# Performance work log

Hardware: AMD Instinct MI355X
Metric: run time of the kernel (lower is better)

Reference implementation:

```python
import jax, jax.numpy as jnp
import numpy as np

BETA = 0.25


def setup_inputs() -> dict:
    key = jax.random.key(0)
    k1, k2 = jax.random.split(key)
    B, D, H, W, K = 16, 256, 32, 32, 8192
    z_e = jax.random.normal(k1, (B, D, H, W), dtype=jnp.float32)
    # codebook init uniform(-1/K, 1/K) as in torch
    codebook = jax.random.uniform(k2, (K, D), dtype=jnp.float32,
                                  minval=-1.0 / K, maxval=1.0 / K)
    return {"z_e": z_e, "codebook": codebook}


def reference(z_e, codebook):
    B, D, H, W = z_e.shape
    K = codebook.shape[0]
    # (B, D, H, W) -> (BHW, D)
    z_flat = jnp.transpose(z_e, (0, 2, 3, 1)).reshape(-1, D)

    # distances computed under no_grad in torch -> stop_gradient here
    zf = jax.lax.stop_gradient(z_flat)
    cb = jax.lax.stop_gradient(codebook)
    # ||z||^2 + ||e||^2 - 2 z.e  -> (BHW, K)
    dist = ((zf * zf).sum(axis=1, keepdims=True)
            + (cb * cb).sum(axis=1)[None, :]
            - 2.0 * (zf @ cb.T))
    indices = jnp.argmin(dist, axis=1)  # (BHW,)

    # embedding gather, reshape back to (B, D, H, W)
    z_q_flat = codebook[indices]
    z_q = jnp.transpose(z_q_flat.reshape(B, H, W, D), (0, 3, 1, 2))

    # straight-through estimator
    z_q_st = z_e + jax.lax.stop_gradient(z_q - z_e)

    codebook_loss = jnp.mean((jax.lax.stop_gradient(z_q) - z_e) ** 2)
    commitment_loss = jnp.mean((z_q - jax.lax.stop_gradient(z_e)) ** 2)
    vq_loss = codebook_loss + BETA * commitment_loss

    # perplexity: one_hot(indices).mean(0) == counts / N
    N = z_flat.shape[0]
    counts = jnp.zeros((K,), dtype=z_flat.dtype).at[indices].add(1.0)
    avg_probs = counts / N
    perplexity = jnp.exp(-jnp.sum(avg_probs * jnp.log(avg_probs + 1e-10)))

    return (z_q_st, vq_loss, indices.reshape(B, H, W), perplexity)
```

## Files before the change

### kernel.cpp

```cpp
#include <hip/hip_runtime.h>

#define DD 256
#define KK 8192
#define HW 1024
#define NROWS 16384
#define NELEM 4194304
#define MT 32
#define MS 64
#define MARGIN 6e-4f
#define WCAP 1024
#define NSLICE 4

typedef __attribute__((ext_vector_type(8))) short short8;
typedef __attribute__((ext_vector_type(4))) float f32x4;
typedef __attribute__((ext_vector_type(4))) unsigned int ux4;
typedef unsigned short ushort;
typedef unsigned int uint;
typedef unsigned long long u64;

__device__ __forceinline__ float np_pw128_sq(const float* p) {
  float r[8];
#pragma unroll
  for (int j = 0; j < 8; ++j) r[j] = __fmul_rn(p[j], p[j]);
  for (int i = 8; i < 128; i += 8) {
#pragma unroll
    for (int j = 0; j < 8; ++j)
      r[j] = __fadd_rn(r[j], __fmul_rn(p[i + j], p[i + j]));
  }
  return __fadd_rn(__fadd_rn(__fadd_rn(r[0], r[1]), __fadd_rn(r[2], r[3])),
                   __fadd_rn(__fadd_rn(r[4], r[5]), __fadd_rn(r[6], r[7])));
}

__device__ __forceinline__ ushort f2bf(float x) {
  uint u = __float_as_uint(x);
  u += 0x7FFF + ((u >> 16) & 1);
  return (ushort)(u >> 16);
}

__device__ __forceinline__ uint fenc(float f) {
  uint u = __float_as_uint(f);
  return (u & 0x80000000u) ? ~u : (u | 0x80000000u);
}
__device__ __forceinline__ float fdec(uint k) {
  return __uint_as_float((k & 0x80000000u) ? (k & 0x7FFFFFFFu) : ~k);
}

struct Top2 { float m1, m2; int i1; };

__device__ __forceinline__ void top2_upd(Top2& s, const f32x4 a,
                                         const f32x4 Bs, int ibase) {
  float d0 = fmaf(-2.f, a[0], Bs[0]);
  float d1 = fmaf(-2.f, a[1], Bs[1]);
  float d2 = fmaf(-2.f, a[2], Bs[2]);
  float d3 = fmaf(-2.f, a[3], Bs[3]);
  float lo01 = fminf(d0, d1), hi01 = fmaxf(d0, d1);
  int io01 = d1 < d0 ? ibase + 1 : ibase;
  float lo23 = fminf(d2, d3), hi23 = fmaxf(d2, d3);
  int io23 = d3 < d2 ? ibase + 3 : ibase + 2;
  float n1 = fminf(lo01, lo23);
  int ni = lo23 < lo01 ? io23 : io01;
  float n2 = fminf(fmaxf(lo01, lo23), fminf(hi01, hi23));
  s.m2 = fminf(fmaxf(s.m1, n1), fminf(s.m2, n2));
  s.i1 = n1 < s.m1 ? ni : s.i1;
  s.m1 = fminf(s.m1, n1);
}

__device__ __forceinline__ void top2_bfly(Top2& s, int off) {
  float om1 = __shfl_xor(s.m1, off);
  int oi1 = __shfl_xor(s.i1, off);
  float om2 = __shfl_xor(s.m2, off);
  s.m2 = fminf(fmaxf(s.m1, om1), fminf(s.m2, om2));
  s.i1 = om1 < s.m1 ? oi1 : s.i1;
  s.m1 = fminf(s.m1, om1);
}

__device__ __forceinline__ uint pack_m2(float m2, int i1) {
  uint u = __float_as_uint(m2);
  uint hi = u & 0xFFFF0000u;
  if ((u & 0x80000000u) && (u & 0xFFFFu)) hi += 0x10000u;
  return hi | (uint)i1;
}

__global__ __launch_bounds__(256) void vq_prep(const float* __restrict__ cb,
                                               float* __restrict__ Bk,
                                               ushort* __restrict__ cbB) {
  const int b = blockIdx.x, t = threadIdx.x;
  if (b < 64) {
    int tid2 = b * 256 + t;
    int k = tid2 >> 1, half = tid2 & 1;
    float h = np_pw128_sq(cb + (size_t)k * DD + half * 128);
    float ho = __shfl_xor(h, 1);
    if (half == 0) Bk[k] = __fadd_rn(h, ho);
  } else {
    int tid = (b - 64) * 256 + t;
    int g = tid >> 9, s = (tid >> 6) & 7, lane = tid & 63;
    int code = g * 16 + (lane & 15);
    int dbase = s * 32 + (lane >> 4) * 8;
    const float* p = cb + (size_t)code * DD + dbase;
    ushort bb[8];
#pragma unroll
    for (int j = 0; j < 8; ++j) bb[j] = f2bf(p[j]);
    uint4 pk;
    pk.x = bb[0] | ((uint)bb[1] << 16);
    pk.y = bb[2] | ((uint)bb[3] << 16);
    pk.z = bb[4] | ((uint)bb[5] << 16);
    pk.w = bb[6] | ((uint)bb[7] << 16);
    *(uint4*)(cbB + (size_t)tid * 8) = pk;
  }
}

#define GG_BODY(BUF, GGI, IB)                                                  \
  {                                                                            \
    f32x4 A0 = {0,0,0,0}, A1 = {0,0,0,0}, A2 = {0,0,0,0}, A3 = {0,0,0,0};      \
    _Pragma("unroll")                                                          \
    for (int s = 0; s < 8; ++s) {                                              \
      A0 = __builtin_amdgcn_mfma_f32_16x16x32_bf16(BUF[s], aF0[s], A0, 0, 0, 0);\
      A1 = __builtin_amdgcn_mfma_f32_16x16x32_bf16(BUF[s], aF1[s], A1, 0, 0, 0);\
      A2 = __builtin_amdgcn_mfma_f32_16x16x32_bf16(BUF[s], aF2[s], A2, 0, 0, 0);\
      A3 = __builtin_amdgcn_mfma_f32_16x16x32_bf16(BUF[s], aF3[s], A3, 0, 0, 0);\
    }                                                                          \
    const f32x4 Bs = *(const f32x4*)(BkS + (GGI) * 16 - cbase + quad * 4);     \
    top2_upd(c0, A0, Bs, IB); top2_upd(c1, A1, Bs, IB);                        \
    top2_upd(c2, A2, Bs, IB); top2_upd(c3, A3, Bs, IB);                        \
  }

__global__ __launch_bounds__(256, 1) void vq_screen(
    const float* __restrict__ z, const ushort* __restrict__ cbB,
    const float* __restrict__ Bk, float* __restrict__ tA,
    uint* __restrict__ tB, uint* __restrict__ rowMinG) {
  __shared__ ushort ztB[MS][264];
  __shared__ float BkS[2048];
  const int bid = blockIdx.x;
  const int rt = bid >> 2, cs = bid & 3;
  const int t = threadIdx.x;
  const int n0 = rt * MS;
  const int bimg = n0 >> 10, hw0 = n0 & 1023;
  const float* zb = z + (size_t)bimg * DD * HW + hw0;

  for (int li = t; li < MS * 128; li += 256) {
    int r = li & 63, dp = li >> 6;
    float v0 = zb[(size_t)(2 * dp) * HW + r];
    float v1 = zb[(size_t)(2 * dp + 1) * HW + r];
    *(uint*)&ztB[r][2 * dp] = (uint)f2bf(v0) | ((uint)f2bf(v1) << 16);
  }
  for (int li = t; li < 2048; li += 256) BkS[li] = Bk[cs * 2048 + li];
  __syncthreads();

  const int w = t >> 6, lane = t & 63;
  const int quad = lane >> 4, n16 = lane & 15;

  short8 aF0[8], aF1[8], aF2[8], aF3[8];
#pragma unroll
  for (int s = 0; s < 8; ++s) {
    aF0[s] = *(const short8*)&ztB[n16][s * 32 + quad * 8];
    aF1[s] = *(const short8*)&ztB[16 + n16][s * 32 + quad * 8];
    aF2[s] = *(const short8*)&ztB[32 + n16][s * 32 + quad * 8];
    aF3[s] = *(const short8*)&ztB[48 + n16][s * 32 + quad * 8];
  }
#pragma unroll
  for (int s = 0; s < 8; ++s) {
    asm volatile("" : "+v"(*(ux4*)&aF0[s]));
    asm volatile("" : "+v"(*(ux4*)&aF1[s]));
    asm volatile("" : "+v"(*(ux4*)&aF2[s]));
    asm volatile("" : "+v"(*(ux4*)&aF3[s]));
  }

  const int gg0 = cs * 128 + w * 32;
  const int cbase = cs * 2048;
  Top2 c0 = {3.4e38f, 3.4e38f, 0}, c1 = {3.4e38f, 3.4e38f, 0};
  Top2 c2 = {3.4e38f, 3.4e38f, 0}, c3 = {3.4e38f, 3.4e38f, 0};
  float rmin = 3.4e38f;

  short8 b0[8], b1[8];
  {
    const ushort* bp = cbB + (size_t)gg0 * 4096 + lane * 8;
#pragma unroll
    for (int s = 0; s < 8; ++s) b0[s] = *(const short8*)(bp + s * 512);
  }

  for (int gp = 0; gp < 16; ++gp) {
    const int gg = gg0 + gp * 2;
    {
      const ushort* bp = cbB + (size_t)(gg + 1) * 4096 + lane * 8;
#pragma unroll
      for (int s = 0; s < 8; ++s) b1[s] = *(const short8*)(bp + s * 512);
    }
    GG_BODY(b0, gg, quad * 4)
    if (gp < 15) {
      const ushort* bp = cbB + (size_t)(gg + 2) * 4096 + lane * 8;
#pragma unroll
      for (int s = 0; s < 8; ++s) b0[s] = *(const short8*)(bp + s * 512);
    }
    GG_BODY(b1, gg + 1, 16 + quad * 4)
    top2_bfly(c0, 16); top2_bfly(c0, 32);
    top2_bfly(c1, 16); top2_bfly(c1, 32);
    top2_bfly(c2, 16); top2_bfly(c2, 32);
    top2_bfly(c3, 16); top2_bfly(c3, 32);
    const size_t tbase = (size_t)(gg >> 1) * NROWS + n0;
    if (quad == 0) {
      __builtin_nontemporal_store(c0.m1, &tA[tbase + n16]);
      __builtin_nontemporal_store(pack_m2(c0.m2, c0.i1), &tB[tbase + n16]);
      rmin = fminf(rmin, c0.m1);
    } else if (quad == 1) {
      __builtin_nontemporal_store(c1.m1, &tA[tbase + 16 + n16]);
      __builtin_nontemporal_store(pack_m2(c1.m2, c1.i1), &tB[tbase + 16 + n16]);
      rmin = fminf(rmin, c1.m1);
    } else if (quad == 2) {
      __builtin_nontemporal_store(c2.m1, &tA[tbase + 32 + n16]);
      __builtin_nontemporal_store(pack_m2(c2.m2, c2.i1), &tB[tbase + 32 + n16]);
      rmin = fminf(rmin, c2.m1);
    } else {
      __builtin_nontemporal_store(c3.m1, &tA[tbase + 48 + n16]);
      __builtin_nontemporal_store(pack_m2(c3.m2, c3.i1), &tB[tbase + 48 + n16]);
      rmin = fminf(rmin, c3.m1);
    }
    c0 = Top2{3.4e38f, 3.4e38f, 0}; c1 = Top2{3.4e38f, 3.4e38f, 0};
    c2 = Top2{3.4e38f, 3.4e38f, 0}; c3 = Top2{3.4e38f, 3.4e38f, 0};
  }
  atomicMin(&rowMinG[n0 + quad * 16 + n16], fenc(rmin));
}

__global__ __launch_bounds__(256) void vq_rerank(
    const float* __restrict__ z, const float* __restrict__ cb,
    const float* __restrict__ Bk, const float* __restrict__ tA,
    const uint* __restrict__ tB, const uint* __restrict__ rowMinG,
    float* __restrict__ out, int* __restrict__ hist,
    float* __restrict__ loss_acc, u64* __restrict__ rowBest) {
  __shared__ float zt[MT][DD + 1];
  __shared__ float thr[MT];
  __shared__ float ArS[MT];
  __shared__ int wl[WCAP];
  __shared__ int wcnt;
  __shared__ int kwin[MT];
  __shared__ float lred[4];

  const int t = threadIdx.x;
  const int n0 = blockIdx.x * MT;
  const int bimg = n0 >> 10, hw0 = n0 & 1023;
  const float* zb = z + (size_t)bimg * DD * HW + hw0;

  if (t == 0) wcnt = 0;
  for (int li = t; li < MT * DD; li += 256) {
    int d = li >> 5, r = li & 31;
    zt[r][d] = zb[d * HW + r];
  }
  __syncthreads();

  const int w = t >> 6, lane = t & 63;

  if (t < MT) {
    thr[t] = fdec(rowMinG[n0 + t]) + MARGIN;
  } else if (t >= 128 && t < 192) {
    int rr = (t - 128) >> 1, half = t & 1;
    float h = np_pw128_sq(&zt[rr][half * 128]);
    float ho = __shfl_xor(h, 1);
    if (half == 0) ArS[rr] = __fadd_rn(h, ho);
  }
  __syncthreads();

  auto exact_one = [&](int rr, int code) {
    const float* cp = cb + (size_t)code * DD;
    float dot = 0.f;
#pragma unroll
    for (int d0 = 0; d0 < DD; d0 += 4) {
      float4 v = *(const float4*)(cp + d0);
      dot = fmaf(zt[rr][d0 + 0], v.x, dot);
      dot = fmaf(zt[rr][d0 + 1], v.y, dot);
      dot = fmaf(zt[rr][d0 + 2], v.z, dot);
      dot = fmaf(zt[rr][d0 + 3], v.w, dot);
    }
    float bd = __fsub_rn(__fadd_rn(ArS[rr], Bk[code]), __fmul_rn(2.f, dot));
    atomicMin(&rowBest[n0 + rr],
              ((u64)__float_as_uint(bd) << 32) | (unsigned)code);
  };

  for (int it = 0; it < 8; ++it) {
    const int li = it * 256 + t;
    const int tile = li >> 3, r4 = (li & 7) << 2;
    const f32x4 a4 = __builtin_nontemporal_load(
        (const f32x4*)&tA[(size_t)tile * NROWS + n0 + r4]);
#pragma unroll
    for (int e = 0; e < 4; ++e) {
      const int rr = r4 + e;
      const float th = thr[rr];
      if (a4[e] <= th) {
        const uint pk = __builtin_nontemporal_load(
            &tB[(size_t)tile * NROWS + n0 + rr]);
        const float m2f = __uint_as_float(pk & 0xFFFF0000u);
        if (m2f <= th) {
          for (int c = 0; c < 32; ++c) {
            int pos = atomicAdd(&wcnt, 1);
            if (pos < WCAP) wl[pos] = (rr << 16) | (tile * 32 + c);
            else exact_one(rr, tile * 32 + c);
          }
        } else {
          int pos = atomicAdd(&wcnt, 1);
          if (pos < WCAP) wl[pos] = (rr << 16) | (tile * 32 + (int)(pk & 31u));
          else exact_one(rr, tile * 32 + (int)(pk & 31u));
        }
      }
    }
  }
  __syncthreads();

  const int cnt = min(wcnt, WCAP);
  for (int e = t; e < cnt; e += 256) {
    const int ent = wl[e];
    exact_one(ent >> 16, ent & 0xFFFF);
  }
  __syncthreads();

  if (t < MT) {
    u64 key = atomicMin(&rowBest[n0 + t], 0xFFFFFFFFFFFFFFFFull);
    int bi = (int)(key & 0xFFFFFFFFull);
    kwin[t] = bi;
    atomicAdd(&hist[bi], 1);
    out[(size_t)NELEM + 1 + n0 + t] = (float)bi;
  }
  __syncthreads();

  float lsum = 0.f;
  for (int it = 0; it < MT * DD / 256; ++it) {
    int li = it * 256 + t;
    int d = li >> 5, rr = li & 31;
    float ze = zt[rr][d];
    float zq = cb[(size_t)kwin[rr] * DD + d];
    float diff = __fsub_rn(zq, ze);
    float st = __fadd_rn(ze, diff);
    out[(size_t)(bimg * DD + d) * HW + hw0 + rr] = st;
    lsum = fmaf(diff, diff, lsum);
  }
#pragma unroll
  for (int off = 32; off > 0; off >>= 1) lsum += __shfl_down(lsum, off);
  if (lane == 0) lred[w] = lsum;
  __syncthreads();
  if (t == 0)
    atomicAdd(loss_acc, ((lred[0] + lred[1]) + (lred[2] + lred[3])));
}

__global__ __launch_bounds__(256) void vq_final(const int* __restrict__ hist,
                                                const float* __restrict__ loss,
                                                float* __restrict__ out) {
  __shared__ float sred[256];
  int t = threadIdx.x;
  float s = 0.f;
  for (int k = t; k < KK; k += 256) {
    float p = (float)hist[k] * (1.f / 16384.f);
    s += p * logf(p + 1e-10f);
  }
  sred[t] = s;
  __syncthreads();
  for (int off = 128; off > 0; off >>= 1) {
    if (t < off) sred[t] += sred[t + off];
    __syncthreads();
  }
  if (t == 0) {
    float L = loss[0] / (float)NELEM;
    out[NELEM] = 1.25f * L;
    out[(size_t)NELEM + 1 + NROWS] = expf(-sred[0]);
  }
}

extern "C" void kernel_launch(void* const* d_in, const int* in_sizes, int n_in,
                              void* d_out, int out_size, void* d_ws, size_t ws_size,
                              hipStream_t stream) {
  const float* z = (const float*)d_in[0];
  const float* cb = (const float*)d_in[1];
  float* out = (float*)d_out;

  float* wsf = (float*)d_ws;
  int* hist = (int*)d_ws;
  float* loss = wsf + 8192;
  float* Bk = wsf + 8448;
  uint* rowMinG = (uint*)(wsf + 16640);
  u64* rowBest = (u64*)(wsf + 33024);
  ushort* cbB = (ushort*)(wsf + 65792);
  float* tA = wsf + 1114368;
  uint* tB = (uint*)(wsf + 5308672);

  hipMemsetAsync(d_ws, 0, 8448 * sizeof(float), stream);
  hipMemsetAsync(wsf + 16640, 0xFF, 196608, stream);
  vq_prep<<<1088, 256, 0, stream>>>(cb, Bk, cbB);
  vq_screen<<<(NROWS / MS) * NSLICE, 256, 0, stream>>>(z, cbB, Bk, tA, tB,
                                                       rowMinG);
  vq_rerank<<<NROWS / MT, 256, 0, stream>>>(z, cb, Bk, tA, tB, rowMinG, out,
                                            hist, loss, rowBest);
  vq_final<<<1, 256, 0, stream>>>(hist, loss, out);
}
```

Before: 221.3 us.

## Fold workspace memsets into prep kernel and keep per-row best in LDS

```diff
diff --git a/kernel.cpp b/kernel.cpp
--- a/kernel.cpp
+++ b/kernel.cpp
@@ -83,7 +83,10 @@
 
 __global__ __launch_bounds__(256) void vq_prep(const float* __restrict__ cb,
                                                float* __restrict__ Bk,
-                                               ushort* __restrict__ cbB) {
+                                               ushort* __restrict__ cbB,
+                                               uint* __restrict__ rowMinG,
+                                               int* __restrict__ hist,
+                                               float* __restrict__ loss) {
   const int b = blockIdx.x, t = threadIdx.x;
   if (b < 64) {
     int tid2 = b * 256 + t;
@@ -91,6 +94,9 @@
     float h = np_pw128_sq(cb + (size_t)k * DD + half * 128);
     float ho = __shfl_xor(h, 1);
     if (half == 0) Bk[k] = __fadd_rn(h, ho);
+    rowMinG[tid2] = 0xFFFFFFFFu;
+    if (b < 32) hist[tid2] = 0;
+    if (tid2 == 0) loss[0] = 0.f;
   } else {
     int tid = (b - 64) * 256 + t;
     int g = tid >> 9, s = (tid >> 6) & 7, lane = tid & 63;
@@ -124,7 +130,8 @@
     top2_upd(c2, A2, Bs, IB); top2_upd(c3, A3, Bs, IB);                        \
   }
 
-__global__ __launch_bounds__(256, 1) void vq_screen(
+__global__ __launch_bounds__(256)
+__attribute__((amdgpu_waves_per_eu(1, 2))) void vq_screen(
     const float* __restrict__ z, const ushort* __restrict__ cbB,
     const float* __restrict__ Bk, float* __restrict__ tA,
     uint* __restrict__ tB, uint* __restrict__ rowMinG) {
@@ -225,12 +232,13 @@
     const float* __restrict__ Bk, const float* __restrict__ tA,
     const uint* __restrict__ tB, const uint* __restrict__ rowMinG,
     float* __restrict__ out, int* __restrict__ hist,
-    float* __restrict__ loss_acc, u64* __restrict__ rowBest) {
+    float* __restrict__ loss_acc) {
   __shared__ float zt[MT][DD + 1];
-  __shared__ float thr[MT];
   __shared__ float ArS[MT];
   __shared__ int wl[WCAP];
   __shared__ int wcnt;
+  __shared__ int ovf;
+  __shared__ u64 rowBestS[MT];
   __shared__ int kwin[MT];
   __shared__ float lred[4];
 
@@ -239,18 +247,56 @@
   const int bimg = n0 >> 10, hw0 = n0 & 1023;
   const float* zb = z + (size_t)bimg * DD * HW + hw0;
 
-  if (t == 0) wcnt = 0;
-  for (int li = t; li < MT * DD; li += 256) {
-    int d = li >> 5, r = li & 31;
-    zt[r][d] = zb[d * HW + r];
-  }
-  __syncthreads();
-
-  const int w = t >> 6, lane = t & 63;
-
-  if (t < MT) {
-    thr[t] = fdec(rowMinG[n0 + t]) + MARGIN;
-  } else if (t >= 128 && t < 192) {
+  if (t == 0) { wcnt = 0; ovf = 0; }
+  if (t < MT) rowBestS[t] = 0xFFFFFFFFFFFFFFFFull;
+  __syncthreads();
+
+  const int r4 = (t & 7) << 2;
+  float th[4];
+#pragma unroll
+  for (int e = 0; e < 4; ++e) th[e] = fdec(rowMinG[n0 + r4 + e]) + MARGIN;
+
+  float zv[32];
+#pragma unroll
+  for (int it = 0; it < 32; ++it) {
+    int li = it * 256 + t;
+    zv[it] = zb[(size_t)(li >> 5) * HW + (li & 31)];
+  }
+
+  for (int it = 0; it < 8; ++it) {
+    const int li = it * 256 + t;
+    const int tile = li >> 3;
+    const f32x4 a4 = __builtin_nontemporal_load(
+        (const f32x4*)&tA[(size_t)tile * NROWS + n0 + r4]);
+#pragma unroll
+    for (int e = 0; e < 4; ++e) {
+      if (a4[e] <= th[e]) {
+        const int rr = r4 + e;
+        const uint pk = __builtin_nontemporal_load(
+            &tB[(size_t)tile * NROWS + n0 + rr]);
+        const float m2f = __uint_as_float(pk & 0xFFFF0000u);
+        if (m2f <= th[e]) {
+          for (int c = 0; c < 32; ++c) {
+            int pos = atomicAdd(&wcnt, 1);
+            if (pos < WCAP) wl[pos] = (rr << 16) | (tile * 32 + c);
+            else ovf = 1;
+          }
+        } else {
+          int pos = atomicAdd(&wcnt, 1);
+          if (pos < WCAP) wl[pos] = (rr << 16) | (tile * 32 + (int)(pk & 31u));
+          else ovf = 1;
+        }
+      }
+    }
+  }
+
+#pragma unroll
+  for (int it = 0; it < 32; ++it) {
+    int li = it * 256 + t;
+    zt[li & 31][li >> 5] = zv[it];
+  }
+  __syncthreads();
+  if (t >= 128 && t < 192) {
     int rr = (t - 128) >> 1, half = t & 1;
     float h = np_pw128_sq(&zt[rr][half * 128]);
     float ho = __shfl_xor(h, 1);
@@ -270,49 +316,39 @@
       dot = fmaf(zt[rr][d0 + 3], v.w, dot);
     }
     float bd = __fsub_rn(__fadd_rn(ArS[rr], Bk[code]), __fmul_rn(2.f, dot));
-    atomicMin(&rowBest[n0 + rr],
-              ((u64)__float_as_uint(bd) << 32) | (unsigned)code);
+    atomicMin(&rowBestS[rr], ((u64)__float_as_uint(bd) << 32) | (unsigned)code);
   };
-
-  for (int it = 0; it < 8; ++it) {
-    const int li = it * 256 + t;
-    const int tile = li >> 3, r4 = (li & 7) << 2;
-    const f32x4 a4 = __builtin_nontemporal_load(
-        (const f32x4*)&tA[(size_t)tile * NROWS + n0 + r4]);
-#pragma unroll
-    for (int e = 0; e < 4; ++e) {
-      const int rr = r4 + e;
-      const float th = thr[rr];
-      if (a4[e] <= th) {
-        const uint pk = __builtin_nontemporal_load(
-            &tB[(size_t)tile * NROWS + n0 + rr]);
-        const float m2f = __uint_as_float(pk & 0xFFFF0000u);
-        if (m2f <= th) {
-          for (int c = 0; c < 32; ++c) {
-            int pos = atomicAdd(&wcnt, 1);
-            if (pos < WCAP) wl[pos] = (rr << 16) | (tile * 32 + c);
-            else exact_one(rr, tile * 32 + c);
-          }
-        } else {
-          int pos = atomicAdd(&wcnt, 1);
-          if (pos < WCAP) wl[pos] = (rr << 16) | (tile * 32 + (int)(pk & 31u));
-          else exact_one(rr, tile * 32 + (int)(pk & 31u));
-        }
-      }
-    }
-  }
-  __syncthreads();
 
   const int cnt = min(wcnt, WCAP);
   for (int e = t; e < cnt; e += 256) {
     const int ent = wl[e];
     exact_one(ent >> 16, ent & 0xFFFF);
   }
-  __syncthreads();
-
+  if (ovf) {
+    for (int it = 0; it < 8; ++it) {
+      const int li = it * 256 + t;
+      const int tile = li >> 3;
+      const f32x4 a4 = *(const f32x4*)&tA[(size_t)tile * NROWS + n0 + r4];
+#pragma unroll
+      for (int e = 0; e < 4; ++e) {
+        if (a4[e] <= th[e]) {
+          const int rr = r4 + e;
+          const uint pk = tB[(size_t)tile * NROWS + n0 + rr];
+          const float m2f = __uint_as_float(pk & 0xFFFF0000u);
+          if (m2f <= th[e]) {
+            for (int c = 0; c < 32; ++c) exact_one(rr, tile * 32 + c);
+          } else {
+            exact_one(rr, tile * 32 + (int)(pk & 31u));
+          }
+        }
+      }
+    }
+  }
+  __syncthreads();
+
+  const int w = t >> 6, lane = t & 63;
   if (t < MT) {
-    u64 key = atomicMin(&rowBest[n0 + t], 0xFFFFFFFFFFFFFFFFull);
-    int bi = (int)(key & 0xFFFFFFFFull);
+    int bi = (int)(rowBestS[t] & 0xFFFFFFFFull);
     kwin[t] = bi;
     atomicAdd(&hist[bi], 1);
     out[(size_t)NELEM + 1 + n0 + t] = (float)bi;
@@ -373,17 +409,14 @@
   float* loss = wsf + 8192;
   float* Bk = wsf + 8448;
   uint* rowMinG = (uint*)(wsf + 16640);
-  u64* rowBest = (u64*)(wsf + 33024);
-  ushort* cbB = (ushort*)(wsf + 65792);
-  float* tA = wsf + 1114368;
-  uint* tB = (uint*)(wsf + 5308672);
-
-  hipMemsetAsync(d_ws, 0, 8448 * sizeof(float), stream);
-  hipMemsetAsync(wsf + 16640, 0xFF, 196608, stream);
-  vq_prep<<<1088, 256, 0, stream>>>(cb, Bk, cbB);
+  ushort* cbB = (ushort*)(wsf + 33024);
+  float* tA = wsf + 1081600;
+  uint* tB = (uint*)(wsf + 5275904);
+
+  vq_prep<<<1088, 256, 0, stream>>>(cb, Bk, cbB, rowMinG, hist, loss);
   vq_screen<<<(NROWS / MS) * NSLICE, 256, 0, stream>>>(z, cbB, Bk, tA, tB,
                                                        rowMinG);
   vq_rerank<<<NROWS / MT, 256, 0, stream>>>(z, cb, Bk, tA, tB, rowMinG, out,
-                                            hist, loss, rowBest);
+                                            hist, loss);
   vq_final<<<1, 256, 0, stream>>>(hist, loss, out);
 }
```

Result: slower. 236.7 us (+6.9%).
